# Optimization experiments

Hardware: AMD Instinct MI355X
Metric: run time of the kernel (lower is better)

The kernel has to match this reference:

```python
import jax, jax.numpy as jnp
import numpy as np

N_EMBD = 1024
N_HEAD = 16
B, T = 4, 2048

def setup_inputs() -> dict:
    key = jax.random.key(0)
    ks = jax.random.split(key, 5)
    s = 0.02
    return {
        "x": jax.random.normal(ks[0], (B, T, N_EMBD), dtype=jnp.float32),
        "w_attn": jax.random.normal(ks[1], (N_EMBD, 3 * N_EMBD), dtype=jnp.float32) * s,
        "b_attn": jnp.zeros((3 * N_EMBD,), dtype=jnp.float32),
        "w_proj": jax.random.normal(ks[2], (N_EMBD, N_EMBD), dtype=jnp.float32) * s,
        "b_proj": jnp.zeros((N_EMBD,), dtype=jnp.float32),
    }

def reference(x, w_attn, b_attn, w_proj, b_proj):
    Bx, Tx, C = x.shape
    hd = C // N_HEAD
    qkv = x @ w_attn + b_attn  # [B,T,3C]
    q, k, v = jnp.split(qkv, 3, axis=-1)
    # [B,H,T,hd]
    q = q.reshape(Bx, Tx, N_HEAD, hd).transpose(0, 2, 1, 3)
    k = k.reshape(Bx, Tx, N_HEAD, hd).transpose(0, 2, 1, 3)
    v = v.reshape(Bx, Tx, N_HEAD, hd).transpose(0, 2, 1, 3)
    scale = 1.0 / np.sqrt(hd).astype(np.float32)
    wei = jnp.einsum('bhqd,bhkd->bhqk', q, k) * scale
    causal = jnp.tril(jnp.ones((Tx, Tx), dtype=bool))
    wei = jnp.where(causal[None, None], wei, jnp.float32(-jnp.inf))
    wei = jax.nn.softmax(wei, axis=-1)
    out = jnp.einsum('bhqk,bhkd->bhqd', wei, v)
    out = out.transpose(0, 2, 1, 3).reshape(Bx, Tx, C)
    return out @ w_proj + b_proj
```

## Files before the change

### kernel.cpp

```cpp
#include <hip/hip_runtime.h>
#include <hip/hip_bf16.h>
#include <math.h>

#define BB 4
#define TT 2048
#define CC 1024
#define HH 16
#define HD 64
#define C3 3072
#define MM (BB * TT)

typedef __attribute__((ext_vector_type(8))) short bf16x8;
typedef __attribute__((ext_vector_type(4))) float f32x4;
typedef __attribute__((ext_vector_type(4))) short s16x4;

__device__ inline short f32_to_bf16_bits(float f) {
    unsigned u = __float_as_uint(f);
    u += 0x7fffu + ((u >> 16) & 1u);
    return (short)(u >> 16);
}

__device__ inline void async_copy16(const void* g, void* l) {
    __builtin_amdgcn_global_load_lds((const __attribute__((address_space(1))) void*)g,
                                     (__attribute__((address_space(3))) void*)l, 16, 0, 0);
}

__global__ __launch_bounds__(256) void cast_x(const float* __restrict__ in,
                                              short* __restrict__ out) {
    int i = (blockIdx.x * 256 + threadIdx.x) * 8;
    float4 a = *(const float4*)(in + i);
    float4 b = *(const float4*)(in + i + 4);
    bf16x8 o;
    o[0] = f32_to_bf16_bits(a.x); o[1] = f32_to_bf16_bits(a.y);
    o[2] = f32_to_bf16_bits(a.z); o[3] = f32_to_bf16_bits(a.w);
    o[4] = f32_to_bf16_bits(b.x); o[5] = f32_to_bf16_bits(b.y);
    o[6] = f32_to_bf16_bits(b.z); o[7] = f32_to_bf16_bits(b.w);
    *(bf16x8*)(out + i) = o;
}

__global__ __launch_bounds__(256) void tcast(const float* __restrict__ w,
                                             short* __restrict__ wt,
                                             int K, int N) {
    __shared__ short tile[64][68];
    const int n0 = blockIdx.x * 64, k0 = blockIdx.y * 64;
    const int tid = threadIdx.x;
#pragma unroll
    for (int it = 0; it < 4; ++it) {
        int idx = it * 1024 + tid * 4;
        int r = idx >> 6, c = idx & 63;
        float4 v = *(const float4*)&w[(size_t)(k0 + r) * N + n0 + c];
        tile[r][c + 0] = f32_to_bf16_bits(v.x);
        tile[r][c + 1] = f32_to_bf16_bits(v.y);
        tile[r][c + 2] = f32_to_bf16_bits(v.z);
        tile[r][c + 3] = f32_to_bf16_bits(v.w);
    }
    __syncthreads();
#pragma unroll
    for (int it = 0; it < 4; ++it) {
        int idx = it * 256 + tid;
        int rr = idx >> 4, kc = (idx & 15) * 4;
        s16x4 o = { tile[kc + 0][rr], tile[kc + 1][rr], tile[kc + 2][rr], tile[kc + 3][rr] };
        *(s16x4*)&wt[(size_t)(n0 + rr) * K + k0 + kc] = o;
    }
}

template <bool QKV>
__global__ __launch_bounds__(256) void gemm128(const short* __restrict__ A,
                                               const short* __restrict__ Bt,
                                               const float* __restrict__ bias,
                                               short* __restrict__ qb,
                                               short* __restrict__ kb,
                                               short* __restrict__ vt,
                                               float* __restrict__ out,
                                               int N, int Kdim) {
    __shared__ __align__(16) short As[128 * 64];
    __shared__ __align__(16) short Bs[128 * 64];
    const int tid = threadIdx.x;
    const int wave = tid >> 6, lane = tid & 63;
    const int quad = lane >> 4, l16 = lane & 15;
    const int wm = wave >> 1, wn = wave & 1;
    const int m0 = blockIdx.y * 128, n0 = blockIdx.x * 128;

    f32x4 acc[4][4] = {};

    for (int k0 = 0; k0 < Kdim; k0 += 64) {
#pragma unroll
        for (int c2 = 0; c2 < 4; ++c2) {
            int g = (wave * 4 + c2) * 64 + lane;
            int row = g >> 3;
            int seg = (g & 7) ^ (row & 7);
            async_copy16(A + (size_t)(m0 + row) * Kdim + k0 + seg * 8, As + g * 8);
            async_copy16(Bt + (size_t)(n0 + row) * Kdim + k0 + seg * 8, Bs + g * 8);
        }
        __syncthreads();
#pragma unroll
        for (int ks = 0; ks < 2; ++ks) {
            bf16x8 af[4], bfv[4];
#pragma unroll
            for (int i = 0; i < 4; ++i) {
                int row = wm * 64 + i * 16 + l16;
                int u = (ks * 4 + quad) ^ (row & 7);
                af[i] = *(const bf16x8*)&As[row * 64 + u * 8];
            }
#pragma unroll
            for (int j = 0; j < 4; ++j) {
                int row = wn * 64 + j * 16 + l16;
                int u = (ks * 4 + quad) ^ (row & 7);
                bfv[j] = *(const bf16x8*)&Bs[row * 64 + u * 8];
            }
#pragma unroll
            for (int i = 0; i < 4; ++i)
#pragma unroll
                for (int j = 0; j < 4; ++j)
                    acc[i][j] = __builtin_amdgcn_mfma_f32_16x16x32_bf16(af[i], bfv[j], acc[i][j], 0, 0, 0);
        }
        __syncthreads();
    }

#pragma unroll
    for (int i = 0; i < 4; ++i)
#pragma unroll
        for (int j = 0; j < 4; ++j) {
            int n = n0 + wn * 64 + j * 16 + l16;
            float bv = bias[n];
            if (QKV) {
                int which = n >> 10, cc = n & 1023;
                int h = cc >> 6, d = cc & 63;
                if (which == 2) {
                    int m_base = m0 + wm * 64 + i * 16 + quad * 4;
                    int bb = m_base >> 11, t0 = m_base & 2047;
                    unsigned p0 = ((unsigned)(unsigned short)f32_to_bf16_bits(acc[i][j][0] + bv)) |
                                  ((unsigned)(unsigned short)f32_to_bf16_bits(acc[i][j][1] + bv) << 16);
                    unsigned p1 = ((unsigned)(unsigned short)f32_to_bf16_bits(acc[i][j][2] + bv)) |
                                  ((unsigned)(unsigned short)f32_to_bf16_bits(acc[i][j][3] + bv) << 16);
                    uint2 pk = {p0, p1};
                    *(uint2*)(vt + (((size_t)bb * HH + h) * HD + d) * TT + t0) = pk;
                } else {
#pragma unroll
                    for (int r = 0; r < 4; ++r) {
                        int m = m0 + wm * 64 + i * 16 + quad * 4 + r;
                        int bb = m >> 11, t = m & 2047;
                        short val = f32_to_bf16_bits((acc[i][j][r] + bv) *
                                                     (which == 0 ? 0.18033688011112042f : 1.0f));
                        size_t off = (((size_t)bb * HH + h) * TT + t) * HD + d;
                        if (which == 0) qb[off] = val;
                        else kb[off] = val;
                    }
                }
            } else {
#pragma unroll
                for (int r = 0; r < 4; ++r) {
                    int m = m0 + wm * 64 + i * 16 + quad * 4 + r;
                    out[(size_t)m * N + n] = acc[i][j][r] + bv;
                }
            }
        }
}

__global__ __launch_bounds__(512, 4) void flash_attn(const short* __restrict__ qb,
                                                     const short* __restrict__ kb,
                                                     const short* __restrict__ vt,
                                                     short* __restrict__ ab) {
    __shared__ __align__(16) short Ksh[2][4096];
    __shared__ __align__(16) short Vsh[2][4096];
    __shared__ __align__(16) float plds[8][16][68];

    const int tid = threadIdx.x;
    const int wave = tid >> 6;
    const int lane = tid & 63;
    const int quad = lane >> 4;
    const int l16 = lane & 15;

    const int bh = blockIdx.y;
    const int i = blockIdx.x;
    const int njt = 32 - 2 * i;
    const int q_lo = i * 128 + wave * 16;
    const int q_hi = (15 - i) * 128 + wave * 16;

    const short* qball = qb + (size_t)bh * TT * HD;
    const short* kball = kb + (size_t)bh * TT * HD;
    const short* vtall = vt + (size_t)bh * HD * TT;

    const int sidx = wave * 64 + lane;
    const int srow = sidx >> 3;
    const int sseg = (sidx & 7) ^ (srow & 7);
    const short* kgsrc = kball + (size_t)srow * HD + sseg * 8;
    const short* vgsrc = vtall + (size_t)srow * TT + sseg * 8;

    bf16x8 qfh[2], qfl[2];
#pragma unroll
    for (int h = 0; h < 2; ++h) {
        qfh[h] = *(const bf16x8*)(qball + (size_t)(q_hi + l16) * HD + h * 32 + quad * 8);
        qfl[h] = *(const bf16x8*)(qball + (size_t)(q_lo + l16) * HD + h * 32 + quad * 8);
    }

    f32x4 o_hi[4] = {}, o_lo[4] = {};
    float ls_hi[4] = {0.f, 0.f, 0.f, 0.f}, ls_lo[4] = {0.f, 0.f, 0.f, 0.f};

    async_copy16(kgsrc, &Ksh[0][wave * 512]);
    async_copy16(vgsrc, &Vsh[0][wave * 512]);

    for (int jt = 0; jt < njt; ++jt) {
        const int buf = jt & 1;
        if (jt + 1 < njt) {
            async_copy16(kgsrc + (size_t)(jt + 1) * 64 * HD, &Ksh[buf ^ 1][wave * 512]);
            async_copy16(vgsrc + (jt + 1) * 64, &Vsh[buf ^ 1][wave * 512]);
            asm volatile("s_waitcnt vmcnt(2)" : : : "memory");
        } else {
            asm volatile("s_waitcnt vmcnt(0)" : : : "memory");
        }
        __builtin_amdgcn_sched_barrier(0);
        __builtin_amdgcn_s_barrier();
        __builtin_amdgcn_sched_barrier(0);

        const int j0 = jt * 64;

        if (j0 <= q_hi + 15) {
            f32x4 s[4];
            __builtin_amdgcn_s_setprio(1);
#pragma unroll
            for (int cb = 0; cb < 4; ++cb) {
                int row = cb * 16 + l16;
                bf16x8 k0 = *(const bf16x8*)&Ksh[buf][(row * 8 + (quad ^ (row & 7))) * 8];
                bf16x8 k1 = *(const bf16x8*)&Ksh[buf][(row * 8 + ((4 + quad) ^ (row & 7))) * 8];
                f32x4 a = {};
                a = __builtin_amdgcn_mfma_f32_16x16x32_bf16(qfh[0], k0, a, 0, 0, 0);
                a = __builtin_amdgcn_mfma_f32_16x16x32_bf16(qfh[1], k1, a, 0, 0, 0);
                s[cb] = a;
            }
            __builtin_amdgcn_s_setprio(0);
            if (j0 + 64 > q_hi) {
#pragma unroll
                for (int cb = 0; cb < 4; ++cb) {
                    int j = j0 + cb * 16 + l16;
#pragma unroll
                    for (int r = 0; r < 4; ++r)
                        if (j > q_hi + quad * 4 + r) s[cb][r] = -1e30f;
                }
            }
#pragma unroll
            for (int cb = 0; cb < 4; ++cb)
#pragma unroll
                for (int r = 0; r < 4; ++r) {
                    float p;
                    asm("v_exp_f32 %0, %1" : "=v"(p) : "v"(s[cb][r]));
                    ls_hi[r] += p;
                    plds[wave][quad * 4 + r][cb * 16 + l16] = p;
                }
            {
                const float* prow = &plds[wave][l16][0];
                f32x4 pr0 = *(const f32x4*)(prow + quad * 8);
                f32x4 pr1 = *(const f32x4*)(prow + quad * 8 + 4);
                f32x4 pr2 = *(const f32x4*)(prow + 32 + quad * 8);
                f32x4 pr3 = *(const f32x4*)(prow + 32 + quad * 8 + 4);
                union { unsigned u[4]; bf16x8 v; } pa0u, pa1u;
                asm("v_cvt_pk_bf16_f32 %0, %1, %2" : "=v"(pa0u.u[0]) : "v"(pr0[0]), "v"(pr0[1]));
                asm("v_cvt_pk_bf16_f32 %0, %1, %2" : "=v"(pa0u.u[1]) : "v"(pr0[2]), "v"(pr0[3]));
                asm("v_cvt_pk_bf16_f32 %0, %1, %2" : "=v"(pa0u.u[2]) : "v"(pr1[0]), "v"(pr1[1]));
                asm("v_cvt_pk_bf16_f32 %0, %1, %2" : "=v"(pa0u.u[3]) : "v"(pr1[2]), "v"(pr1[3]));
                asm("v_cvt_pk_bf16_f32 %0, %1, %2" : "=v"(pa1u.u[0]) : "v"(pr2[0]), "v"(pr2[1]));
                asm("v_cvt_pk_bf16_f32 %0, %1, %2" : "=v"(pa1u.u[1]) : "v"(pr2[2]), "v"(pr2[3]));
                asm("v_cvt_pk_bf16_f32 %0, %1, %2" : "=v"(pa1u.u[2]) : "v"(pr3[0]), "v"(pr3[1]));
                asm("v_cvt_pk_bf16_f32 %0, %1, %2" : "=v"(pa1u.u[3]) : "v"(pr3[2]), "v"(pr3[3]));
                bf16x8 pa0 = pa0u.v, pa1 = pa1u.v;
                __builtin_amdgcn_s_setprio(1);
#pragma unroll
                for (int db = 0; db < 4; ++db) {
                    int row = db * 16 + l16;
                    bf16x8 v0 = *(const bf16x8*)&Vsh[buf][(row * 8 + (quad ^ (row & 7))) * 8];
                    bf16x8 v1 = *(const bf16x8*)&Vsh[buf][(row * 8 + ((4 + quad) ^ (row & 7))) * 8];
                    o_hi[db] = __builtin_amdgcn_mfma_f32_16x16x32_bf16(pa0, v0, o_hi[db], 0, 0, 0);
                    o_hi[db] = __builtin_amdgcn_mfma_f32_16x16x32_bf16(pa1, v1, o_hi[db], 0, 0, 0);
                }
                __builtin_amdgcn_s_setprio(0);
            }
        }

        if (j0 <= q_lo + 15) {
            f32x4 s[4];
            __builtin_amdgcn_s_setprio(1);
#pragma unroll
            for (int cb = 0; cb < 4; ++cb) {
                int row = cb * 16 + l16;
                bf16x8 k0 = *(const bf16x8*)&Ksh[buf][(row * 8 + (quad ^ (row & 7))) * 8];
                bf16x8 k1 = *(const bf16x8*)&Ksh[buf][(row * 8 + ((4 + quad) ^ (row & 7))) * 8];
                f32x4 a = {};
                a = __builtin_amdgcn_mfma_f32_16x16x32_bf16(qfl[0], k0, a, 0, 0, 0);
                a = __builtin_amdgcn_mfma_f32_16x16x32_bf16(qfl[1], k1, a, 0, 0, 0);
                s[cb] = a;
            }
            __builtin_amdgcn_s_setprio(0);
            if (j0 + 64 > q_lo) {
#pragma unroll
                for (int cb = 0; cb < 4; ++cb) {
                    int j = j0 + cb * 16 + l16;
#pragma unroll
                    for (int r = 0; r < 4; ++r)
                        if (j > q_lo + quad * 4 + r) s[cb][r] = -1e30f;
                }
            }
#pragma unroll
            for (int cb = 0; cb < 4; ++cb)
#pragma unroll
                for (int r = 0; r < 4; ++r) {
                    float p;
                    asm("v_exp_f32 %0, %1" : "=v"(p) : "v"(s[cb][r]));
                    ls_lo[r] += p;
                    plds[wave][quad * 4 + r][cb * 16 + l16] = p;
                }
            {
                const float* prow = &plds[wave][l16][0];
                f32x4 pr0 = *(const f32x4*)(prow + quad * 8);
                f32x4 pr1 = *(const f32x4*)(prow + quad * 8 + 4);
                f32x4 pr2 = *(const f32x4*)(prow + 32 + quad * 8);
                f32x4 pr3 = *(const f32x4*)(prow + 32 + quad * 8 + 4);
                union { unsigned u[4]; bf16x8 v; } pa0u, pa1u;
                asm("v_cvt_pk_bf16_f32 %0, %1, %2" : "=v"(pa0u.u[0]) : "v"(pr0[0]), "v"(pr0[1]));
                asm("v_cvt_pk_bf16_f32 %0, %1, %2" : "=v"(pa0u.u[1]) : "v"(pr0[2]), "v"(pr0[3]));
                asm("v_cvt_pk_bf16_f32 %0, %1, %2" : "=v"(pa0u.u[2]) : "v"(pr1[0]), "v"(pr1[1]));
                asm("v_cvt_pk_bf16_f32 %0, %1, %2" : "=v"(pa0u.u[3]) : "v"(pr1[2]), "v"(pr1[3]));
                asm("v_cvt_pk_bf16_f32 %0, %1, %2" : "=v"(pa1u.u[0]) : "v"(pr2[0]), "v"(pr2[1]));
                asm("v_cvt_pk_bf16_f32 %0, %1, %2" : "=v"(pa1u.u[1]) : "v"(pr2[2]), "v"(pr2[3]));
                asm("v_cvt_pk_bf16_f32 %0, %1, %2" : "=v"(pa1u.u[2]) : "v"(pr3[0]), "v"(pr3[1]));
                asm("v_cvt_pk_bf16_f32 %0, %1, %2" : "=v"(pa1u.u[3]) : "v"(pr3[2]), "v"(pr3[3]));
                bf16x8 pa0 = pa0u.v, pa1 = pa1u.v;
                __builtin_amdgcn_s_setprio(1);
#pragma unroll
                for (int db = 0; db < 4; ++db) {
                    int row = db * 16 + l16;
                    bf16x8 v0 = *(const bf16x8*)&Vsh[buf][(row * 8 + (quad ^ (row & 7))) * 8];
                    bf16x8 v1 = *(const bf16x8*)&Vsh[buf][(row * 8 + ((4 + quad) ^ (row & 7))) * 8];
                    o_lo[db] = __builtin_amdgcn_mfma_f32_16x16x32_bf16(pa0, v0, o_lo[db], 0, 0, 0);
                    o_lo[db] = __builtin_amdgcn_mfma_f32_16x16x32_bf16(pa1, v1, o_lo[db], 0, 0, 0);
                }
                __builtin_amdgcn_s_setprio(0);
            }
        }
        __builtin_amdgcn_sched_barrier(0);
        __builtin_amdgcn_s_barrier();
    }

    const int b = bh >> 4, hd0 = (bh & 15) * HD;
    float inv_h[4], inv_l[4];
#pragma unroll
    for (int r = 0; r < 4; ++r) {
        float th = ls_hi[r], tl = ls_lo[r];
#pragma unroll
        for (int off = 1; off < 16; off <<= 1) {
            th += __shfl_xor(th, off, 64);
            tl += __shfl_xor(tl, off, 64);
        }
        inv_h[r] = 1.0f / th;
        inv_l[r] = 1.0f / tl;
    }
#pragma unroll
    for (int r = 0; r < 4; ++r) {
        int qh = q_hi + quad * 4 + r;
        int ql = q_lo + quad * 4 + r;
#pragma unroll
        for (int db = 0; db < 4; ++db) {
            ab[((size_t)(b * TT + qh)) * CC + hd0 + db * 16 + l16] =
                f32_to_bf16_bits(o_hi[db][r] * inv_h[r]);
            ab[((size_t)(b * TT + ql)) * CC + hd0 + db * 16 + l16] =
                f32_to_bf16_bits(o_lo[db][r] * inv_l[r]);
        }
    }
}

extern "C" void kernel_launch(void* const* d_in, const int* in_sizes, int n_in,
                              void* d_out, int out_size, void* d_ws, size_t ws_size,
                              hipStream_t stream) {
    const float* x      = (const float*)d_in[0];
    const float* w_attn = (const float*)d_in[1];
    const float* b_attn = (const float*)d_in[2];
    const float* w_proj = (const float*)d_in[3];
    const float* b_proj = (const float*)d_in[4];
    float* out = (float*)d_out;

    const size_t per = (size_t)BB * HH * TT * HD;
    short* xb      = (short*)d_ws;
    short* wt_attn = xb + per;
    short* wt_proj = wt_attn + (size_t)C3 * CC;
    short* qb      = wt_proj + (size_t)CC * CC;
    short* kb      = qb + per;
    short* vt      = kb + per;
    short* ab      = vt + per;

    cast_x<<<dim3(MM * CC / (256 * 8)), 256, 0, stream>>>(x, xb);
    tcast<<<dim3(C3 / 64, CC / 64), 256, 0, stream>>>(w_attn, wt_attn, CC, C3);
    tcast<<<dim3(CC / 64, CC / 64), 256, 0, stream>>>(w_proj, wt_proj, CC, CC);

    gemm128<true><<<dim3(C3 / 128, MM / 128), 256, 0, stream>>>(
        xb, wt_attn, b_attn, qb, kb, vt, nullptr, C3, CC);

    flash_attn<<<dim3(8, BB * HH), 512, 0, stream>>>(qb, kb, vt, ab);

    gemm128<false><<<dim3(CC / 128, MM / 128), 256, 0, stream>>>(
        ab, wt_proj, b_proj, nullptr, nullptr, nullptr, out, CC, CC);
}
```

Measured before the change: 168.8 us.

## Replace QKV GEMM with 256x256 tile, 8-wave kernel using interleaved async LDS pipeline

Result: slower. 185.9 us (+10.1%).

```diff
diff --git a/kernel.cpp b/kernel.cpp
--- a/kernel.cpp
+++ b/kernel.cpp
@@ -64,13 +64,9 @@
     }
 }
 
-template <bool QKV>
 __global__ __launch_bounds__(256) void gemm128(const short* __restrict__ A,
                                                const short* __restrict__ Bt,
                                                const float* __restrict__ bias,
-                                               short* __restrict__ qb,
-                                               short* __restrict__ kb,
-                                               short* __restrict__ vt,
                                                float* __restrict__ out,
                                                int N, int Kdim) {
     __shared__ __align__(16) short As[128 * 64];
@@ -123,35 +119,146 @@
         for (int j = 0; j < 4; ++j) {
             int n = n0 + wn * 64 + j * 16 + l16;
             float bv = bias[n];
-            if (QKV) {
-                int which = n >> 10, cc = n & 1023;
-                int h = cc >> 6, d = cc & 63;
-                if (which == 2) {
-                    int m_base = m0 + wm * 64 + i * 16 + quad * 4;
-                    int bb = m_base >> 11, t0 = m_base & 2047;
-                    unsigned p0 = ((unsigned)(unsigned short)f32_to_bf16_bits(acc[i][j][0] + bv)) |
-                                  ((unsigned)(unsigned short)f32_to_bf16_bits(acc[i][j][1] + bv) << 16);
-                    unsigned p1 = ((unsigned)(unsigned short)f32_to_bf16_bits(acc[i][j][2] + bv)) |
-                                  ((unsigned)(unsigned short)f32_to_bf16_bits(acc[i][j][3] + bv) << 16);
-                    uint2 pk = {p0, p1};
-                    *(uint2*)(vt + (((size_t)bb * HH + h) * HD + d) * TT + t0) = pk;
-                } else {
-#pragma unroll
-                    for (int r = 0; r < 4; ++r) {
-                        int m = m0 + wm * 64 + i * 16 + quad * 4 + r;
-                        int bb = m >> 11, t = m & 2047;
-                        short val = f32_to_bf16_bits((acc[i][j][r] + bv) *
-                                                     (which == 0 ? 0.18033688011112042f : 1.0f));
-                        size_t off = (((size_t)bb * HH + h) * TT + t) * HD + d;
-                        if (which == 0) qb[off] = val;
-                        else kb[off] = val;
-                    }
-                }
+#pragma unroll
+            for (int r = 0; r < 4; ++r) {
+                int m = m0 + wm * 64 + i * 16 + quad * 4 + r;
+                out[(size_t)m * N + n] = acc[i][j][r] + bv;
+            }
+        }
+}
+
+#define BAR() { asm volatile("" ::: "memory"); __builtin_amdgcn_s_barrier(); asm volatile("" ::: "memory"); }
+
+#define STAGE_A(t, h) { \
+    short* d_ = &As[(t) & 1][(h) * 8192]; \
+    const short* s_ = A + ((t) * 64 + (h) * 32); \
+    async_copy16(s_ + offA0, d_ + ldst0); \
+    async_copy16(s_ + offA1, d_ + ldst1); }
+
+#define STAGE_B(t, h) { \
+    short* d_ = &Bs[(t) & 1][(h) * 8192]; \
+    const short* s_ = Bt + ((t) * 64 + (h) * 32); \
+    async_copy16(s_ + offB0, d_ + ldst0); \
+    async_copy16(s_ + offB1, d_ + ldst1); }
+
+#define LOAD_AF(buf, h, mh) { \
+    const short* Ab_ = &As[buf][(h) * 8192 + ardbase + (mh) * 2048]; \
+    af[0] = *(const bf16x8*)&Ab_[0];    af[1] = *(const bf16x8*)&Ab_[512]; \
+    af[2] = *(const bf16x8*)&Ab_[1024]; af[3] = *(const bf16x8*)&Ab_[1536]; }
+
+#define LOAD_BF(buf, h) { \
+    const short* Bb_ = &Bs[buf][(h) * 8192 + brdbase]; \
+    bf[0] = *(const bf16x8*)&Bb_[0];    bf[1] = *(const bf16x8*)&Bb_[512]; \
+    bf[2] = *(const bf16x8*)&Bb_[1024]; bf[3] = *(const bf16x8*)&Bb_[1536]; }
+
+#define MFMA16(mh) { \
+    __builtin_amdgcn_s_setprio(1); \
+    _Pragma("unroll") for (int f_ = 0; f_ < 4; ++f_) \
+    _Pragma("unroll") for (int j_ = 0; j_ < 4; ++j_) \
+        acc[(mh) * 4 + f_][j_] = __builtin_amdgcn_mfma_f32_16x16x32_bf16(af[f_], bf[j_], acc[(mh) * 4 + f_][j_], 0, 0, 0); \
+    __builtin_amdgcn_s_setprio(0); }
+
+__global__ __launch_bounds__(512, 2) void gemm256_qkv(const short* __restrict__ A,
+                                                      const short* __restrict__ Bt,
+                                                      const float* __restrict__ bias,
+                                                      short* __restrict__ qb,
+                                                      short* __restrict__ kb,
+                                                      short* __restrict__ vt) {
+    __shared__ __align__(16) short As[2][16384];
+    __shared__ __align__(16) short Bs[2][16384];
+    const int tid = threadIdx.x;
+    const int w = tid >> 6, lane = tid & 63;
+    const int quad = lane >> 4, l16 = lane & 15;
+    const int wm = w >> 2, wn = w & 3;
+
+    const int id = blockIdx.y * 12 + blockIdx.x;
+    const int swz = (id & 7) * 48 + (id >> 3);
+    const int bx = swz % 12, by = swz / 12;
+    const int m0 = by * 256, n0 = bx * 256;
+
+    const int srow = w * 32 + (lane >> 2);
+    const int sseg = (lane & 3) * 8;
+    const size_t offA0 = (size_t)(m0 + srow) * 1024 + sseg;
+    const size_t offA1 = offA0 + (size_t)16 * 1024;
+    const size_t offB0 = (size_t)(n0 + srow) * 1024 + sseg;
+    const size_t offB1 = offB0 + (size_t)16 * 1024;
+    const int ldst0 = (w * 128 + lane) * 8;
+    const int ldst1 = ldst0 + 512;
+
+    const int ardbase = (wm * 128 + l16) * 32 + quad * 8;
+    const int brdbase = (wn * 64 + l16) * 32 + quad * 8;
+
+    f32x4 acc[8][4] = {};
+    bf16x8 af[4], bf[4];
+
+    STAGE_A(0, 0); STAGE_B(0, 0); STAGE_A(0, 1); STAGE_B(0, 1);
+    STAGE_A(1, 0); STAGE_B(1, 0);
+    asm volatile("s_waitcnt vmcnt(4)" ::: "memory");
+    BAR();
+
+#pragma unroll 1
+    for (int it = 0; it < 8; ++it) {
+        const int t0 = 2 * it;
+        const bool pf = (it + 1 < 8);
+        LOAD_AF(0, 0, 0); LOAD_BF(0, 0);
+        STAGE_A(t0 + 1, 1);
+        BAR(); MFMA16(0); BAR();
+        LOAD_AF(0, 0, 1);
+        STAGE_B(t0 + 1, 1);
+        BAR(); MFMA16(1); BAR();
+        LOAD_AF(0, 1, 0); LOAD_BF(0, 1);
+        if (pf) STAGE_A(t0 + 2, 0);
+        BAR(); MFMA16(0); BAR();
+        LOAD_AF(0, 1, 1);
+        if (pf) STAGE_B(t0 + 2, 0);
+        BAR(); MFMA16(1);
+        if (pf) { asm volatile("s_waitcnt vmcnt(4)" ::: "memory"); }
+        else    { asm volatile("s_waitcnt vmcnt(0)" ::: "memory"); }
+        BAR();
+        LOAD_AF(1, 0, 0); LOAD_BF(1, 0);
+        if (pf) STAGE_A(t0 + 2, 1);
+        BAR(); MFMA16(0); BAR();
+        LOAD_AF(1, 0, 1);
+        if (pf) STAGE_B(t0 + 2, 1);
+        BAR(); MFMA16(1); BAR();
+        LOAD_AF(1, 1, 0); LOAD_BF(1, 1);
+        if (pf) STAGE_A(t0 + 3, 0);
+        BAR(); MFMA16(0); BAR();
+        LOAD_AF(1, 1, 1);
+        if (pf) STAGE_B(t0 + 3, 0);
+        BAR(); MFMA16(1);
+        asm volatile("s_waitcnt vmcnt(4)" ::: "memory");
+        BAR();
+    }
+
+#pragma unroll
+    for (int f = 0; f < 8; ++f)
+#pragma unroll
+        for (int j = 0; j < 4; ++j) {
+            int n = n0 + wn * 64 + j * 16 + l16;
+            float bv = bias[n];
+            int which = n >> 10, cc = n & 1023;
+            int hh = cc >> 6, d = cc & 63;
+            f32x4 v = acc[f][j];
+            if (which == 2) {
+                int m_base = m0 + wm * 128 + f * 16 + quad * 4;
+                int bb = m_base >> 11, t0v = m_base & 2047;
+                unsigned p0 = ((unsigned)(unsigned short)f32_to_bf16_bits(v[0] + bv)) |
+                              ((unsigned)(unsigned short)f32_to_bf16_bits(v[1] + bv) << 16);
+                unsigned p1 = ((unsigned)(unsigned short)f32_to_bf16_bits(v[2] + bv)) |
+                              ((unsigned)(unsigned short)f32_to_bf16_bits(v[3] + bv) << 16);
+                uint2 pk = {p0, p1};
+                *(uint2*)(vt + (((size_t)bb * HH + hh) * HD + d) * TT + t0v) = pk;
             } else {
 #pragma unroll
                 for (int r = 0; r < 4; ++r) {
-                    int m = m0 + wm * 64 + i * 16 + quad * 4 + r;
-                    out[(size_t)m * N + n] = acc[i][j][r] + bv;
+                    int m = m0 + wm * 128 + f * 16 + quad * 4 + r;
+                    int bb = m >> 11, t = m & 2047;
+                    short val = f32_to_bf16_bits((v[r] + bv) *
+                                                 (which == 0 ? 0.18033688011112042f : 1.0f));
+                    size_t off = (((size_t)bb * HH + hh) * TT + t) * HD + d;
+                    if (which == 0) qb[off] = val;
+                    else kb[off] = val;
                 }
             }
         }
@@ -390,11 +497,11 @@
     tcast<<<dim3(C3 / 64, CC / 64), 256, 0, stream>>>(w_attn, wt_attn, CC, C3);
     tcast<<<dim3(CC / 64, CC / 64), 256, 0, stream>>>(w_proj, wt_proj, CC, CC);
 
-    gemm128<true><<<dim3(C3 / 128, MM / 128), 256, 0, stream>>>(
-        xb, wt_attn, b_attn, qb, kb, vt, nullptr, C3, CC);
+    gemm256_qkv<<<dim3(C3 / 256, MM / 256), 512, 0, stream>>>(
+        xb, wt_attn, b_attn, qb, kb, vt);
 
     flash_attn<<<dim3(8, BB * HH), 512, 0, stream>>>(qb, kb, vt, ab);
 
-    gemm128<false><<<dim3(CC / 128, MM / 128), 256, 0, stream>>>(
-        ab, wt_proj, b_proj, nullptr, nullptr, nullptr, out, CC, CC);
-}
+    gemm128<<<dim3(CC / 128, MM / 128), 256, 0, stream>>>(
+        ab, wt_proj, b_proj, out, CC, CC);
+}
```
